# Kernel tuning notes

Measured on AMD Instinct MI355X. Metric: run time of the kernel, lower is better.

Reference implementation:

```python
import jax, jax.numpy as jnp
import numpy as np

DIM = 1024
H = 16
DH = DIM // H  # 64
B = 2
T = 2048
LEFT, RIGHT = 128, 128  # attention_window
CAUSAL = True
SCALE = 1.0 / float(np.sqrt(DH))


def rotate_half(x):
    x1, x2 = jnp.split(x, 2, axis=-1)
    return jnp.concatenate((-x2, x1), axis=-1)


def apply_rotary_pos_emb(pos, t):
    # pos: [b, t, dh] -> [b, 1, t, dh]; t: [b, h, t, dh]
    pos = pos[:, None]
    return t * jnp.cos(pos) + rotate_half(t) * jnp.sin(pos)


def setup_inputs() -> dict:
    key = jax.random.key(0)
    ks = jax.random.split(key, 6)
    s = 1.0 / np.sqrt(DIM)
    x = jax.random.normal(ks[0], (B, T, DIM), dtype=jnp.float32)
    attention_mask = jnp.ones((T, T), dtype=bool)
    rotary_emb = jax.random.normal(ks[1], (B, T, DH), dtype=jnp.float32)
    Wq = jax.random.normal(ks[2], (DIM, DIM), dtype=jnp.float32) * s
    Wk = jax.random.normal(ks[3], (DIM, DIM), dtype=jnp.float32) * s
    Wv = jax.random.normal(ks[4], (DIM, DIM), dtype=jnp.float32) * s
    Wo = jax.random.normal(ks[5], (DIM, DIM), dtype=jnp.float32) * s
    return {"x": x, "attention_mask": attention_mask, "rotary_emb": rotary_emb,
            "Wq": Wq, "Wk": Wk, "Wv": Wv, "Wo": Wo}


def _build_mask(attention_mask):
    # i = key/column index, j = query/row index (matches torch code)
    i = jnp.arange(T)[None, :]
    j = jnp.arange(T)[:, None]
    mask = (i >= j - LEFT) & (i <= j + RIGHT)  # sliding window
    if CAUSAL:
        mask = mask & (i <= j)  # tril
    return attention_mask & mask  # [T, T]


def reference(x, attention_mask, rotary_emb, Wq, Wk, Wv, Wo):
    b, t, d = x.shape
    # QKV projections (nn.Linear: x @ W.T), split heads: b t (h dh) -> b h t dh
    def proj(W):
        return (x @ W.T).reshape(b, t, H, DH).transpose(0, 2, 1, 3)
    q, k, v = proj(Wq), proj(Wk), proj(Wv)
    q = apply_rotary_pos_emb(rotary_emb, q)
    k = apply_rotary_pos_emb(rotary_emb, k)
    mask = _build_mask(attention_mask)  # [T, T]
    scores = jnp.einsum('bhqd,bhkd->bhqk', q, k) * SCALE
    neg = jnp.asarray(-1e9, scores.dtype)
    scores = jnp.where(mask, scores, neg)
    attn = jax.nn.softmax(scores, axis=-1)
    out = jnp.einsum('bhqk,bhkd->bhqd', attn, v)
    out = out.transpose(0, 2, 1, 3).reshape(b, t, d)  # b h t dh -> b t (h dh)
    return out @ Wo.T
```

## Files before the change

kernel.cpp:

```cpp
#include <hip/hip_runtime.h>
#include <hip/hip_bf16.h>
#include <cstdint>

#define DIMD 1024
#define NH 16
#define DHD 64
#define BB 2
#define TT 2048
#define MROWS (BB * TT)

typedef unsigned short u16;
typedef unsigned int u32;
typedef __attribute__((ext_vector_type(8))) __bf16 bf16x8;
typedef __attribute__((ext_vector_type(4))) float f32x4;

__device__ __forceinline__ u16 f2bf(float f) {
    union { float f; unsigned int i; } v; v.f = f;
    unsigned int u = v.i;
    unsigned int r = (u + 0x7fffu + ((u >> 16) & 1u)) >> 16;
    return (u16)r;
}
__device__ __forceinline__ int4 pack8(const float4& a, const float4& b) {
    union { int4 v; u16 u[8]; } t;
    t.u[0] = f2bf(a.x); t.u[1] = f2bf(a.y); t.u[2] = f2bf(a.z); t.u[3] = f2bf(a.w);
    t.u[4] = f2bf(b.x); t.u[5] = f2bf(b.y); t.u[6] = f2bf(b.z); t.u[7] = f2bf(b.w);
    return t.v;
}

__global__ __launch_bounds__(256) void convert_all(const float* __restrict__ x,
                                                   const float* __restrict__ Wq,
                                                   const float* __restrict__ Wk,
                                                   const float* __restrict__ Wv,
                                                   const float* __restrict__ Wo,
                                                   u16* __restrict__ xb,
                                                   u16* __restrict__ wqkv,
                                                   u16* __restrict__ wob) {
    int t = blockIdx.x * 256 + threadIdx.x;
    const float* src; u16* dst; int rel;
    if (t < 524288)      { src = x;  dst = xb;             rel = t; }
    else if (t < 655360) { src = Wq; dst = wqkv;           rel = t - 524288; }
    else if (t < 786432) { src = Wk; dst = wqkv + 1048576; rel = t - 655360; }
    else if (t < 917504) { src = Wv; dst = wqkv + 2097152; rel = t - 786432; }
    else                 { src = Wo; dst = wob;            rel = t - 917504; }
    size_t e = (size_t)rel * 8;
    float4 a = *(const float4*)(src + e);
    float4 b = *(const float4*)(src + e + 4);
    *(int4*)(dst + e) = pack8(a, b);
}

__global__ __launch_bounds__(256) void gemm_qkv(const u16* __restrict__ xb,
                                                const u16* __restrict__ wqkv,
                                                u16* __restrict__ qb,
                                                u16* __restrict__ kb,
                                                u16* __restrict__ vbT,
                                                const float* __restrict__ rot) {
    constexpr int Kd = 1024;
    __shared__ u16 As[2][128 * 32];
    __shared__ u16 Bs[2][128 * 32];

    const int tid  = threadIdx.x;
    const int lane = tid & 63;
    const int w    = tid >> 6;
    const int m0   = blockIdx.y * 128;
    const int n0   = blockIdx.x * 128;

    const u16* Ag = xb   + (size_t)(m0 + 32 * w + (lane >> 2)) * Kd + (lane & 3) * 8;
    const u16* Bg = wqkv + (size_t)(n0 + 32 * w + (lane >> 2)) * Kd + (lane & 3) * 8;
    const int soff0 = (32 * w + (lane >> 2)) * 32 + (lane & 3) * 8;
    const int soff1 = soff0 + 16 * 32;

    const int r16  = lane & 15;
    const int quad = lane >> 4;
    const int q8   = quad * 8;
    const int wm   = (w >> 1) * 64;
    const int wn   = (w & 1) * 64;

    f32x4 acc[4][4];
#pragma unroll
    for (int i = 0; i < 4; i++)
#pragma unroll
        for (int j = 0; j < 4; j++) acc[i][j] = f32x4{0.f, 0.f, 0.f, 0.f};

    int4 a0, a1, b0, b1;
    auto loadregs = [&](int k) {
        a0 = *(const int4*)(Ag + k);
        a1 = *(const int4*)(Ag + 16 * Kd + k);
        b0 = *(const int4*)(Bg + k);
        b1 = *(const int4*)(Bg + 16 * Kd + k);
    };
    auto writebuf = [&](int buf) {
        *(int4*)&As[buf][soff0] = a0;
        *(int4*)&As[buf][soff1] = a1;
        *(int4*)&Bs[buf][soff0] = b0;
        *(int4*)&Bs[buf][soff1] = b1;
    };
    auto compute = [&](int buf) {
        bf16x8 af[4], bfr[4];
#pragma unroll
        for (int i = 0; i < 4; i++)
            af[i] = *(const bf16x8*)&As[buf][(wm + i * 16 + r16) * 32 + q8];
#pragma unroll
        for (int j = 0; j < 4; j++)
            bfr[j] = *(const bf16x8*)&Bs[buf][(wn + j * 16 + r16) * 32 + q8];
#pragma unroll
        for (int mi = 0; mi < 4; mi++)
#pragma unroll
            for (int ni = 0; ni < 4; ni++)
                acc[mi][ni] = __builtin_amdgcn_mfma_f32_16x16x32_bf16(
                    af[mi], bfr[ni], acc[mi][ni], 0, 0, 0);
    };

    loadregs(0);
    writebuf(0);
    __syncthreads();

#pragma unroll 1
    for (int k0 = 0; k0 < Kd; k0 += 64) {
        loadregs(k0 + 32);
        compute(0);
        writebuf(1);
        __syncthreads();
        if (k0 + 64 < Kd) loadregs(k0 + 64);
        compute(1);
        if (k0 + 64 < Kd) {
            writebuf(0);
            __syncthreads();
        }
    }

    const int wsel = n0 >> 10;
    const int nloc = (n0 & 1023) + wn;

    if (wsel < 2) {
        u16* C = (wsel == 0) ? qb : kb;
#pragma unroll
        for (int mi = 0; mi < 4; mi++)
#pragma unroll
            for (int r = 0; r < 4; r++) {
                int row = m0 + wm + mi * 16 + quad * 4 + r;
#pragma unroll
                for (int ni = 0; ni < 2; ni++) {
                    int d = ni * 16 + r16;
                    float s0, c0, s1, c1;
                    __sincosf(rot[row * DHD + d], &s0, &c0);
                    __sincosf(rot[row * DHD + d + 32], &s1, &c1);
                    float x0 = acc[mi][ni][r], x1 = acc[mi][ni + 2][r];
                    C[(size_t)row * DIMD + nloc + d]      = f2bf(x0 * c0 - x1 * s0);
                    C[(size_t)row * DIMD + nloc + d + 32] = f2bf(x1 * c1 + x0 * s1);
                }
            }
    } else {
#pragma unroll
        for (int mi = 0; mi < 4; mi++)
#pragma unroll
            for (int ni = 0; ni < 4; ni++)
#pragma unroll
                for (int r = 0; r < 4; r++) {
                    int row = m0 + wm + mi * 16 + quad * 4 + r;
                    int b   = row >> 11;
                    int t   = row & (TT - 1);
                    int col = nloc + ni * 16 + r16;
                    int h   = col >> 6;
                    int d   = col & 63;
                    vbT[((size_t)(b * NH + h) * DHD + d) * TT + t] =
                        f2bf(acc[mi][ni][r]);
                }
    }
}

__global__ __launch_bounds__(256) void attn_kernel(const u16* __restrict__ Q,
                                                   const u16* __restrict__ K,
                                                   const u16* __restrict__ vbT,
                                                   u16* __restrict__ O) {
    constexpr int LDK = 72;
    constexpr int LDV = 200;
    __shared__ u16 Ks[192 * LDK];
    __shared__ u16 VTs[64 * LDV];
    __shared__ u16 Ps[4 * 16 * LDV];

    const int tid = threadIdx.x;
    const int L   = tid & 63;
    const int w   = tid >> 6;
    const int b   = blockIdx.z;
    const int h   = blockIdx.y;
    const int q0  = blockIdx.x * 64;
    const int kstart = q0 - 128;

    for (int i = tid; i < 1536; i += 256) {
        int kr = i >> 3, c = (i & 7) * 8;
        int kk = kstart + kr;
        int4 val = make_int4(0, 0, 0, 0);
        if (kk >= 0)
            val = *(const int4*)&K[(size_t)(b * TT + kk) * DIMD + h * DHD + c];
        *(int4*)&Ks[kr * LDK + c] = val;
    }
    for (int i = tid; i < 1536; i += 256) {
        int d = i / 24;
        int c = (i % 24) * 8;
        int kk = kstart + c;
        int4 val = make_int4(0, 0, 0, 0);
        if (kk >= 0)
            val = *(const int4*)&vbT[((size_t)(b * NH + h) * DHD + d) * TT + kk];
        *(int4*)&VTs[d * LDV + c] = val;
    }

    const int r16  = L & 15;
    const int quad = L >> 4;
    const int q8   = quad * 8;

    const size_t qrow = (size_t)(b * TT + q0 + w * 16 + r16) * DIMD + h * DHD;
    bf16x8 aq0 = *(const bf16x8*)&Q[qrow + q8];
    bf16x8 aq1 = *(const bf16x8*)&Q[qrow + 32 + q8];

    __syncthreads();

    float st[12][4];
    float rmax[4] = {-1e30f, -1e30f, -1e30f, -1e30f};
    const float SC = 0.125f;

#pragma unroll
    for (int kt = 0; kt < 12; kt++) {
        bf16x8 bk0 = *(const bf16x8*)&Ks[(kt * 16 + r16) * LDK + q8];
        bf16x8 bk1 = *(const bf16x8*)&Ks[(kt * 16 + r16) * LDK + 32 + q8];
        f32x4 s = f32x4{0.f, 0.f, 0.f, 0.f};
        s = __builtin_amdgcn_mfma_f32_16x16x32_bf16(aq0, bk0, s, 0, 0, 0);
        s = __builtin_amdgcn_mfma_f32_16x16x32_bf16(aq1, bk1, s, 0, 0, 0);
        int ka = kstart + kt * 16 + r16;
#pragma unroll
        for (int r = 0; r < 4; r++) {
            int qa = q0 + w * 16 + quad * 4 + r;
            float sv = s[r] * SC;
            bool ok = (ka >= 0) && (ka <= qa) && (ka >= qa - 128);
            sv = ok ? sv : -1e30f;
            st[kt][r] = sv;
            rmax[r] = fmaxf(rmax[r], sv);
        }
    }
#pragma unroll
    for (int off = 8; off >= 1; off >>= 1)
#pragma unroll
        for (int r = 0; r < 4; r++)
            rmax[r] = fmaxf(rmax[r], __shfl_xor(rmax[r], off, 64));

    u16* Pw = &Ps[w * 16 * LDV];
    float rsum[4] = {0.f, 0.f, 0.f, 0.f};
#pragma unroll
    for (int kt = 0; kt < 12; kt++)
#pragma unroll
        for (int r = 0; r < 4; r++) {
            float p = __expf(st[kt][r] - rmax[r]);
            rsum[r] += p;
            Pw[(quad * 4 + r) * LDV + kt * 16 + r16] = f2bf(p);
        }
#pragma unroll
    for (int off = 8; off >= 1; off >>= 1)
#pragma unroll
        for (int r = 0; r < 4; r++)
            rsum[r] += __shfl_xor(rsum[r], off, 64);
    float rinv[4];
#pragma unroll
    for (int r = 0; r < 4; r++) rinv[r] = 1.0f / rsum[r];

    __syncthreads();

    bf16x8 pa[6];
#pragma unroll
    for (int kc = 0; kc < 6; kc++)
        pa[kc] = *(const bf16x8*)&Pw[r16 * LDV + kc * 32 + q8];

#pragma unroll
    for (int nt = 0; nt < 4; nt++) {
        f32x4 acc = f32x4{0.f, 0.f, 0.f, 0.f};
#pragma unroll
        for (int kc = 0; kc < 6; kc++) {
            bf16x8 bv = *(const bf16x8*)&VTs[(nt * 16 + r16) * LDV + kc * 32 + q8];
            acc = __builtin_amdgcn_mfma_f32_16x16x32_bf16(pa[kc], bv, acc, 0, 0, 0);
        }
#pragma unroll
        for (int r = 0; r < 4; r++) {
            int qa = q0 + w * 16 + quad * 4 + r;
            O[(size_t)(b * TT + qa) * DIMD + h * DHD + nt * 16 + r16] =
                f2bf(acc[r] * rinv[r]);
        }
    }
}

__global__ __launch_bounds__(256) void gemm_out(const u16* __restrict__ A,
                                                const u16* __restrict__ Wb,
                                                float* __restrict__ C) {
    constexpr int Kd = 1024, Nd = 1024;
    __shared__ u16 As[2][64 * 32];
    __shared__ u16 Bs[2][128 * 32];

    const int tid  = threadIdx.x;
    const int lane = tid & 63;
    const int w    = tid >> 6;
    const int m0   = blockIdx.y * 64;
    const int n0   = blockIdx.x * 128;

    const u16* Ag = A  + (size_t)(m0 + 16 * w + (lane >> 2)) * Kd + (lane & 3) * 8;
    const u16* Bg = Wb + (size_t)(n0 + 32 * w + (lane >> 2)) * Kd + (lane & 3) * 8;
    const int aoff  = (16 * w + (lane >> 2)) * 32 + (lane & 3) * 8;
    const int boff0 = (32 * w + (lane >> 2)) * 32 + (lane & 3) * 8;
    const int boff1 = boff0 + 16 * 32;

    const int r16  = lane & 15;
    const int quad = lane >> 4;
    const int q8   = quad * 8;
    const int cb   = (w >> 1) * 64 + (w & 1) * 16;

    f32x4 acc[4][2];
#pragma unroll
    for (int i = 0; i < 4; i++)
#pragma unroll
        for (int j = 0; j < 2; j++) acc[i][j] = f32x4{0.f, 0.f, 0.f, 0.f};

    int4 a0, b0, b1;
    auto loadregs = [&](int k) {
        a0 = *(const int4*)(Ag + k);
        b0 = *(const int4*)(Bg + k);
        b1 = *(const int4*)(Bg + 16 * Kd + k);
    };
    auto writebuf = [&](int buf) {
        *(int4*)&As[buf][aoff]  = a0;
        *(int4*)&Bs[buf][boff0] = b0;
        *(int4*)&Bs[buf][boff1] = b1;
    };
    auto compute = [&](int buf) {
        bf16x8 af[4], bfr[2];
#pragma unroll
        for (int i = 0; i < 4; i++)
            af[i] = *(const bf16x8*)&As[buf][(i * 16 + r16) * 32 + q8];
#pragma unroll
        for (int j = 0; j < 2; j++)
            bfr[j] = *(const bf16x8*)&Bs[buf][(cb + j * 32 + r16) * 32 + q8];
#pragma unroll
        for (int mi = 0; mi < 4; mi++)
#pragma unroll
            for (int ni = 0; ni < 2; ni++)
                acc[mi][ni] = __builtin_amdgcn_mfma_f32_16x16x32_bf16(
                    af[mi], bfr[ni], acc[mi][ni], 0, 0, 0);
    };

    loadregs(0);
    writebuf(0);
    __syncthreads();

#pragma unroll 1
    for (int k0 = 0; k0 < Kd; k0 += 64) {
        loadregs(k0 + 32);
        compute(0);
        writebuf(1);
        __syncthreads();
        if (k0 + 64 < Kd) loadregs(k0 + 64);
        compute(1);
        if (k0 + 64 < Kd) {
            writebuf(0);
            __syncthreads();
        }
    }

#pragma unroll
    for (int mi = 0; mi < 4; mi++)
#pragma unroll
        for (int j = 0; j < 2; j++)
#pragma unroll
            for (int r = 0; r < 4; r++) {
                int row = m0 + mi * 16 + quad * 4 + r;
                C[(size_t)row * Nd + n0 + cb + j * 32 + r16] = acc[mi][j][r];
            }
}

extern "C" void kernel_launch(void* const* d_in, const int* in_sizes, int n_in,
                              void* d_out, int out_size, void* d_ws, size_t ws_size,
                              hipStream_t stream) {
    const float* x   = (const float*)d_in[0];
    const float* rot = (const float*)d_in[2];
    const float* Wq  = (const float*)d_in[3];
    const float* Wk  = (const float*)d_in[4];
    const float* Wv  = (const float*)d_in[5];
    const float* Wo  = (const float*)d_in[6];
    float* out = (float*)d_out;

    u16* xb   = (u16*)d_ws;
    u16* wqkv = xb + 4194304;
    u16* wob  = wqkv + 3145728;
    u16* qb   = wob + 1048576;
    u16* kb   = qb + 4194304;
    u16* vbT  = kb + 4194304;
    u16* ab   = vbT + 4194304;

    convert_all<<<4096, 256, 0, stream>>>(x, Wq, Wk, Wv, Wo, xb, wqkv, wob);
    gemm_qkv<<<dim3(3 * DIMD / 128, MROWS / 128), 256, 0, stream>>>(
        xb, wqkv, qb, kb, vbT, rot);
    attn_kernel<<<dim3(TT / 64, NH, BB), 256, 0, stream>>>(qb, kb, vbT, ab);
    gemm_out<<<dim3(DIMD / 128, MROWS / 64), 256, 0, stream>>>(ab, wob, out);
}
```

Before: 170.0 us.

## Deepen GEMM global prefetch to two stages and alias attention P buffer onto K tile

```diff
diff --git a/kernel.cpp b/kernel.cpp
--- a/kernel.cpp
+++ b/kernel.cpp
@@ -81,18 +81,18 @@
 #pragma unroll
         for (int j = 0; j < 4; j++) acc[i][j] = f32x4{0.f, 0.f, 0.f, 0.f};
 
-    int4 a0, a1, b0, b1;
-    auto loadregs = [&](int k) {
-        a0 = *(const int4*)(Ag + k);
-        a1 = *(const int4*)(Ag + 16 * Kd + k);
-        b0 = *(const int4*)(Bg + k);
-        b1 = *(const int4*)(Bg + 16 * Kd + k);
-    };
-    auto writebuf = [&](int buf) {
-        *(int4*)&As[buf][soff0] = a0;
-        *(int4*)&As[buf][soff1] = a1;
-        *(int4*)&Bs[buf][soff0] = b0;
-        *(int4*)&Bs[buf][soff1] = b1;
+    int4 ra[2][2], rb[2][2];
+    auto loadset = [&](int s, int k) {
+        ra[s][0] = *(const int4*)(Ag + k);
+        ra[s][1] = *(const int4*)(Ag + 16 * Kd + k);
+        rb[s][0] = *(const int4*)(Bg + k);
+        rb[s][1] = *(const int4*)(Bg + 16 * Kd + k);
+    };
+    auto writebuf = [&](int s, int buf) {
+        *(int4*)&As[buf][soff0] = ra[s][0];
+        *(int4*)&As[buf][soff1] = ra[s][1];
+        *(int4*)&Bs[buf][soff0] = rb[s][0];
+        *(int4*)&Bs[buf][soff1] = rb[s][1];
     };
     auto compute = [&](int buf) {
         bf16x8 af[4], bfr[4];
@@ -110,20 +110,21 @@
                     af[mi], bfr[ni], acc[mi][ni], 0, 0, 0);
     };
 
-    loadregs(0);
-    writebuf(0);
+    loadset(0, 0);
+    writebuf(0, 0);
+    loadset(1, 32);
     __syncthreads();
 
 #pragma unroll 1
     for (int k0 = 0; k0 < Kd; k0 += 64) {
-        loadregs(k0 + 32);
+        if (k0 + 64 < Kd) loadset(0, k0 + 64);
         compute(0);
-        writebuf(1);
+        writebuf(1, 1);
         __syncthreads();
-        if (k0 + 64 < Kd) loadregs(k0 + 64);
+        if (k0 + 96 < Kd) loadset(1, k0 + 96);
         compute(1);
         if (k0 + 64 < Kd) {
-            writebuf(0);
+            writebuf(0, 0);
             __syncthreads();
         }
     }
@@ -176,7 +177,6 @@
     constexpr int LDV = 200;
     __shared__ u16 Ks[192 * LDK];
     __shared__ u16 VTs[64 * LDV];
-    __shared__ u16 Ps[4 * 16 * LDV];
 
     const int tid = threadIdx.x;
     const int L   = tid & 63;
@@ -242,7 +242,9 @@
         for (int r = 0; r < 4; r++)
             rmax[r] = fmaxf(rmax[r], __shfl_xor(rmax[r], off, 64));
 
-    u16* Pw = &Ps[w * 16 * LDV];
+    __syncthreads();
+
+    u16* Pw = &Ks[w * 16 * LDV];
     float rsum[4] = {0.f, 0.f, 0.f, 0.f};
 #pragma unroll
     for (int kt = 0; kt < 12; kt++)
@@ -315,16 +317,16 @@
 #pragma unroll
         for (int j = 0; j < 2; j++) acc[i][j] = f32x4{0.f, 0.f, 0.f, 0.f};
 
-    int4 a0, b0, b1;
-    auto loadregs = [&](int k) {
-        a0 = *(const int4*)(Ag + k);
-        b0 = *(const int4*)(Bg + k);
-        b1 = *(const int4*)(Bg + 16 * Kd + k);
-    };
-    auto writebuf = [&](int buf) {
-        *(int4*)&As[buf][aoff]  = a0;
-        *(int4*)&Bs[buf][boff0] = b0;
-        *(int4*)&Bs[buf][boff1] = b1;
+    int4 ra[2], rb[2][2];
+    auto loadset = [&](int s, int k) {
+        ra[s]    = *(const int4*)(Ag + k);
+        rb[s][0] = *(const int4*)(Bg + k);
+        rb[s][1] = *(const int4*)(Bg + 16 * Kd + k);
+    };
+    auto writebuf = [&](int s, int buf) {
+        *(int4*)&As[buf][aoff]  = ra[s];
+        *(int4*)&Bs[buf][boff0] = rb[s][0];
+        *(int4*)&Bs[buf][boff1] = rb[s][1];
     };
     auto compute = [&](int buf) {
         bf16x8 af[4], bfr[2];
@@ -342,20 +344,21 @@
                     af[mi], bfr[ni], acc[mi][ni], 0, 0, 0);
     };
 
-    loadregs(0);
-    writebuf(0);
+    loadset(0, 0);
+    writebuf(0, 0);
+    loadset(1, 32);
     __syncthreads();
 
 #pragma unroll 1
     for (int k0 = 0; k0 < Kd; k0 += 64) {
-        loadregs(k0 + 32);
+        if (k0 + 64 < Kd) loadset(0, k0 + 64);
         compute(0);
-        writebuf(1);
+        writebuf(1, 1);
         __syncthreads();
-        if (k0 + 64 < Kd) loadregs(k0 + 64);
+        if (k0 + 96 < Kd) loadset(1, k0 + 96);
         compute(1);
         if (k0 + 64 < Kd) {
-            writebuf(0);
+            writebuf(0, 0);
             __syncthreads();
         }
     }
```

New measurement: 308.6 us. 81.5% more time.
